# Optimization experiments

Hardware: AMD Instinct MI355X
Metric: run time of the kernel (lower is better)

Reference implementation:

```python
import jax, jax.numpy as jnp
import numpy as np

N_SRC, N_DST, E, D, H = 100000, 10000, 320000, 128, 128
LN_EPS = 1e-5


def setup_inputs() -> dict:
    key = jax.random.key(0)
    ks = jax.random.split(key, 12)
    h_src = jax.random.normal(ks[0], (N_SRC, D), jnp.float32)
    h_dst = jax.random.normal(ks[1], (N_DST, D), jnp.float32)
    s_emb = jax.random.normal(ks[2], (N_DST, D), jnp.float32)
    edge_weight = jax.random.uniform(ks[3], (E,), jnp.float32)
    src_idx = jax.random.randint(ks[4], (E,), 0, N_SRC)
    dst_idx = jnp.sort(jax.random.randint(ks[5], (E,), 0, N_DST))
    # session_attention: Linear(2D->H, no bias) -> tanh -> Linear(H->1, no bias)
    W1 = jax.random.normal(ks[6], (2 * D, H), jnp.float32) / np.sqrt(2 * D)
    w2 = jax.random.normal(ks[7], (H,), jnp.float32) / np.sqrt(H)
    # output_proj: Linear(2D->D) with bias
    Wo = jax.random.normal(ks[8], (2 * D, D), jnp.float32) / np.sqrt(2 * D)
    bo = jnp.zeros((D,), jnp.float32)
    gamma = jnp.ones((D,), jnp.float32)
    beta = jnp.zeros((D,), jnp.float32)
    return {"h_src": h_src, "h_dst": h_dst, "s_emb": s_emb,
            "edge_weight": edge_weight, "src_idx": src_idx, "dst_idx": dst_idx,
            "W1": W1, "w2": w2, "Wo": Wo, "bo": bo, "gamma": gamma, "beta": beta}


def reference(h_src, h_dst, s_emb, edge_weight, src_idx, dst_idx, W1, w2, Wo, bo, gamma, beta):
    d = h_src.shape[1]
    # concat([h_src[src], s_emb[dst]]) @ W1 == h_src[src] @ W1[:d] + s_emb[dst] @ W1[d:]
    # project per-node first (cheaper than per-edge concat matmul)
    p_src = h_src @ W1[:d]          # [N_src, H]
    p_dst = s_emb @ W1[d:]          # [N_dst, H]
    raw = jnp.tanh(p_src[src_idx] + p_dst[dst_idx]) @ w2   # [E]
    raw = raw * edge_weight
    # edge_softmax: segment softmax over incoming edges of each dst node
    seg_max = jax.ops.segment_max(raw, dst_idx, num_segments=h_dst.shape[0])
    seg_max = jnp.where(jnp.isfinite(seg_max), seg_max, 0.0)  # handle degree-0 dsts
    ex = jnp.exp(raw - seg_max[dst_idx])
    den = jax.ops.segment_sum(ex, dst_idx, num_segments=h_dst.shape[0])
    attn = ex / den[dst_idx]                                 # [E]
    # u_mul_e + sum: weighted gather-scatter aggregation
    h_global = jax.ops.segment_sum(h_src[src_idx] * attn[:, None], dst_idx,
                                   num_segments=h_dst.shape[0])  # [N_dst, D]
    # output_proj on concat([h_dst, h_global])
    out = h_dst @ Wo[:d] + h_global @ Wo[d:] + bo
    # residual + layer norm (dropout = identity in eval)
    x = h_dst + out
    mu = jnp.mean(x, axis=-1, keepdims=True)
    var = jnp.mean((x - mu) ** 2, axis=-1, keepdims=True)
    y = (x - mu) / jnp.sqrt(var + LN_EPS) * gamma + beta
    return (y, attn[:, None])
```

## Files before the change

### kernel.cpp

```cpp
#include <hip/hip_runtime.h>
#include <math.h>

#define D128 128
#define SCAPW 256

typedef unsigned int uint32;
typedef unsigned short ushort_t;
typedef short bf16x8 __attribute__((ext_vector_type(8)));
typedef float f32x4 __attribute__((ext_vector_type(4)));
typedef float f32x2 __attribute__((ext_vector_type(2)));

__device__ __forceinline__ ushort_t bf16_of(float x) {
  uint32 u = __float_as_uint(x);
  return (ushort_t)((u + 0x7fffu + ((u >> 16) & 1u)) >> 16);
}
__device__ __forceinline__ uint32 pack_bf2(float x, float y) {
  uint32 bx = __float_as_uint(x);
  uint32 by = __float_as_uint(y);
  bx = (bx + 0x7fffu + ((bx >> 16) & 1u)) >> 16;
  by = (by + 0x7fffu + ((by >> 16) & 1u)) & 0xffff0000u;
  return bx | by;
}

__device__ __forceinline__ float fast_tanh(float x) {
  float e = __expf(2.0f * x);
  float r = __builtin_amdgcn_rcpf(1.0f + e);
  return fmaf(-2.0f, r, 1.0f);
}

__device__ __forceinline__ uint32 pack_fp8x4(float a, float b, float c, float d) {
  int u = __builtin_amdgcn_cvt_pk_fp8_f32(a, b, 0, false);
  u = __builtin_amdgcn_cvt_pk_fp8_f32(c, d, u, true);
  return (uint32)u;
}

__device__ __forceinline__ bf16x8 bf16x8_of(float4 a, float4 c) {
  union { uint4 u; bf16x8 h; } r;
  r.u.x = pack_bf2(a.x, a.y);
  r.u.y = pack_bf2(a.z, a.w);
  r.u.z = pack_bf2(c.x, c.y);
  r.u.w = pack_bf2(c.z, c.w);
  return r.h;
}

__global__ __launch_bounds__(256) void prep_all(
    const float* __restrict__ W1, const float* __restrict__ Wo,
    const int* __restrict__ dst_idx,
    ushort_t* __restrict__ Wfrag, ushort_t* __restrict__ Wo_frag,
    int* __restrict__ off, int E, int N) {
  const int b = blockIdx.x;
  const int tid = threadIdx.x;
  if (b < 16) {
    int t = b * 256 + tid;
    int lane = t & 63;
    int kc = (t >> 6) & 3;
    int nt = (t >> 8) & 7;
    int h = (t >> 11) & 1;
    int m = lane & 15;
    int quad = lane >> 4;
    int krow = h * D128 + kc * 32 + quad * 8;
    int ncol = nt * 16 + m;
    ushort_t fr[8];
#pragma unroll
    for (int j = 0; j < 8; j++) fr[j] = bf16_of(W1[(size_t)(krow + j) * D128 + ncol]);
    *(uint4*)(Wfrag + (size_t)t * 8) = *(const uint4*)fr;
  } else if (b < 32) {
    int t = (b - 16) * 256 + tid;
    int lane = t & 63;
    int kc = (t >> 6) & 7;
    int nt = (t >> 9) & 7;
    int m = lane & 15;
    int quad = lane >> 4;
    int krow = kc * 32 + quad * 8;
    int ncol = nt * 16 + m;
    ushort_t fr[8];
#pragma unroll
    for (int j = 0; j < 8; j++) fr[j] = bf16_of(Wo[(size_t)(krow + j) * D128 + ncol]);
    *(uint4*)(Wo_frag + (size_t)t * 8) = *(const uint4*)fr;
  } else {
    int e = (b - 32) * 256 + tid;
    if (e >= E) return;
    int d = dst_idx[e];
    int dprev = (e == 0) ? -1 : dst_idx[e - 1];
    for (int v = dprev + 1; v <= d; v++) off[v] = e;
    if (e == E - 1) {
      for (int v = d + 1; v <= N; v++) off[v] = E;
    }
  }
}

__global__ __launch_bounds__(256) void gemm_mfma(
    const float* __restrict__ Xa, const float* __restrict__ Xb,
    const ushort_t* __restrict__ Wfrag,
    uint32* __restrict__ Pa, uint32* __restrict__ Pb,
    uint32* __restrict__ x_f8,
    int Ma, int Mb, int nblk_a) {
  __shared__ uint32 Ys8[128][36];
  const int blk = blockIdx.x;
  const float* X;
  const bf16x8* Wf;
  uint32* P;
  int M, row0;
  bool emit8;
  if (blk < nblk_a) {
    X = Xa; P = Pa; Wf = (const bf16x8*)Wfrag;           M = Ma; row0 = blk * 128; emit8 = true;
  } else {
    X = Xb; P = Pb; Wf = (const bf16x8*)(Wfrag + 16384); M = Mb; row0 = (blk - nblk_a) * 128; emit8 = false;
  }

  const int tid = threadIdx.x;
  const int wave = tid >> 6;
  const int lane = tid & 63;
  const int m = lane & 15;
  const int quad = lane >> 4;

  const int ra0 = min(row0 + wave * 32 + m, M - 1);
  const int ra1 = min(row0 + wave * 32 + 16 + m, M - 1);

  f32x4 acc[2][8];
#pragma unroll
  for (int st = 0; st < 2; st++)
#pragma unroll
    for (int nt = 0; nt < 8; nt++) acc[st][nt] = (f32x4){0.f, 0.f, 0.f, 0.f};

#pragma unroll
  for (int kc = 0; kc < 4; kc++) {
    const float* p0 = X + (size_t)ra0 * D128 + kc * 32 + quad * 8;
    const float* p1 = X + (size_t)ra1 * D128 + kc * 32 + quad * 8;
    float4 a0 = *(const float4*)p0;
    float4 a1 = *(const float4*)(p0 + 4);
    float4 b0 = *(const float4*)p1;
    float4 b1 = *(const float4*)(p1 + 4);
    bf16x8 x0 = bf16x8_of(a0, a1);
    bf16x8 x1 = bf16x8_of(b0, b1);
    if (emit8) {
      uint2 q;
      q.x = pack_fp8x4(a0.x, a0.y, a0.z, a0.w);
      q.y = pack_fp8x4(a1.x, a1.y, a1.z, a1.w);
      *(uint2*)(x_f8 + (size_t)ra0 * 32 + kc * 8 + quad * 2) = q;
      q.x = pack_fp8x4(b0.x, b0.y, b0.z, b0.w);
      q.y = pack_fp8x4(b1.x, b1.y, b1.z, b1.w);
      *(uint2*)(x_f8 + (size_t)ra1 * 32 + kc * 8 + quad * 2) = q;
    }
#pragma unroll
    for (int nt = 0; nt < 8; nt++) {
      bf16x8 wf = Wf[(nt * 4 + kc) * 64 + lane];
      acc[0][nt] = __builtin_amdgcn_mfma_f32_16x16x32_bf16(wf, x0, acc[0][nt], 0, 0, 0);
      acc[1][nt] = __builtin_amdgcn_mfma_f32_16x16x32_bf16(wf, x1, acc[1][nt], 0, 0, 0);
    }
  }

#pragma unroll
  for (int st = 0; st < 2; st++)
#pragma unroll
    for (int nt = 0; nt < 8; nt++)
      Ys8[wave * 32 + st * 16 + m][nt * 4 + quad] =
          pack_fp8x4(acc[st][nt][0], acc[st][nt][1], acc[st][nt][2], acc[st][nt][3]);
  __syncthreads();

#pragma unroll
  for (int it = 0; it < 4; it++) {
    int f = tid + 256 * it;
    int row = f >> 3;
    int cu = (f & 7) * 4;
    int grow = row0 + row;
    if (grow < M) *(uint4*)(P + (size_t)grow * 32 + cu) = *(const uint4*)(&Ys8[row][cu]);
  }
}

__global__ __launch_bounds__(256) void attn_agg_kernel(
    const uint32* __restrict__ p_src_f8, const uint32* __restrict__ p_dst_f8,
    const float* __restrict__ w2, const float* __restrict__ ew,
    const int* __restrict__ src_idx, const int* __restrict__ off,
    const uint32* __restrict__ h_src_f8,
    float* __restrict__ attn_out, uint32* __restrict__ h_glob_bf, int N_dst) {
  const int tid = threadIdx.x;
  const int wv = tid >> 6;
  const int lane = tid & 63;
  const int v = blockIdx.x * 4 + wv;

  __shared__ float sex[4][SCAPW];
  __shared__ int ssrc[4][SCAPW];
  if (v >= N_dst) return;

  const int lo = off[v], hi = off[v + 1];
  const int deg = hi - lo;
  const int sub = lane & 15;
  const int eg = lane >> 4;
  const bool fast = (deg <= SCAPW);

  float4 wA = *(const float4*)(w2 + sub * 8);
  float4 wB = *(const float4*)(w2 + sub * 8 + 4);
  uint2 pdu = *(const uint2*)(p_dst_f8 + (size_t)v * 32 + sub * 2);
  f32x2 pd0 = __builtin_amdgcn_cvt_pk_f32_fp8(pdu.x, false);
  f32x2 pd1 = __builtin_amdgcn_cvt_pk_f32_fp8(pdu.x, true);
  f32x2 pd2 = __builtin_amdgcn_cvt_pk_f32_fp8(pdu.y, false);
  f32x2 pd3 = __builtin_amdgcn_cvt_pk_f32_fp8(pdu.y, true);

  float den = 0.f;
  for (int base = 0; base < deg; base += 4) {
    const int ei = base + eg;
    float ex = 0.f;
    if (ei < deg) {
      const int e = lo + ei;
      const int s = src_idx[e];
      const float ewv = ew[e];
      uint2 us = *(const uint2*)(p_src_f8 + (size_t)s * 32 + sub * 2);
      f32x2 a0 = __builtin_amdgcn_cvt_pk_f32_fp8(us.x, false);
      f32x2 a1 = __builtin_amdgcn_cvt_pk_f32_fp8(us.x, true);
      f32x2 a2 = __builtin_amdgcn_cvt_pk_f32_fp8(us.y, false);
      f32x2 a3 = __builtin_amdgcn_cvt_pk_f32_fp8(us.y, true);
      float sc;
      sc = fast_tanh(a0.x + pd0.x) * wA.x;
      sc = fmaf(fast_tanh(a0.y + pd0.y), wA.y, sc);
      sc = fmaf(fast_tanh(a1.x + pd1.x), wA.z, sc);
      sc = fmaf(fast_tanh(a1.y + pd1.y), wA.w, sc);
      sc = fmaf(fast_tanh(a2.x + pd2.x), wB.x, sc);
      sc = fmaf(fast_tanh(a2.y + pd2.y), wB.y, sc);
      sc = fmaf(fast_tanh(a3.x + pd3.x), wB.z, sc);
      sc = fmaf(fast_tanh(a3.y + pd3.y), wB.w, sc);
#pragma unroll
      for (int o = 1; o <= 8; o <<= 1) sc += __shfl_xor(sc, o, 64);
      ex = __expf(sc * ewv);
      if (sub == 0) {
        if (fast) { sex[wv][ei] = ex; ssrc[wv][ei] = s; }
        else attn_out[lo + ei] = ex;
      }
    }
    den += (sub == 0) ? ex : 0.f;
  }
#pragma unroll
  for (int o = 1; o <= 32; o <<= 1) den += __shfl_xor(den, o, 64);
  const float inv = (deg > 0) ? 1.0f / den : 0.0f;

  const int c4 = lane & 31;
  const int hw = lane >> 5;
  float a0 = 0.f, a1 = 0.f, a2 = 0.f, a3 = 0.f;

  if (fast) {
    const int pad = (deg + 15) & ~15;
    for (int i = deg + lane; i < pad; i += 64) { sex[wv][i] = 0.f; ssrc[wv][i] = 0; }
    for (int i = lane; i < deg; i += 64) attn_out[lo + i] = sex[wv][i] * inv;
    for (int b = 0; b < pad; b += 16) {
#pragma unroll
      for (int j = 0; j < 8; j++) {
        const int idx = b + j * 2 + hw;
        float ex = sex[wv][idx];
        int s = ssrc[wv][idx];
        uint32 u = h_src_f8[(size_t)s * 32 + c4];
        f32x2 h0 = __builtin_amdgcn_cvt_pk_f32_fp8(u, false);
        f32x2 h1 = __builtin_amdgcn_cvt_pk_f32_fp8(u, true);
        a0 = fmaf(ex, h0.x, a0);
        a1 = fmaf(ex, h0.y, a1);
        a2 = fmaf(ex, h1.x, a2);
        a3 = fmaf(ex, h1.y, a3);
      }
    }
  } else {
    for (int b = 0; b < deg; b += 16) {
#pragma unroll
      for (int j = 0; j < 8; j++) {
        const int idx = b + j * 2 + hw;
        float ex = 0.f;
        int s = 0;
        if (idx < deg) { ex = attn_out[lo + idx]; s = src_idx[lo + idx]; }
        uint32 u = h_src_f8[(size_t)s * 32 + c4];
        f32x2 h0 = __builtin_amdgcn_cvt_pk_f32_fp8(u, false);
        f32x2 h1 = __builtin_amdgcn_cvt_pk_f32_fp8(u, true);
        a0 = fmaf(ex, h0.x, a0);
        a1 = fmaf(ex, h0.y, a1);
        a2 = fmaf(ex, h1.x, a2);
        a3 = fmaf(ex, h1.y, a3);
      }
    }
    for (int i = lane; i < deg; i += 64) attn_out[lo + i] *= inv;
  }

  a0 += __shfl_xor(a0, 32, 64);
  a1 += __shfl_xor(a1, 32, 64);
  a2 += __shfl_xor(a2, 32, 64);
  a3 += __shfl_xor(a3, 32, 64);
  if (hw == 0) {
    uint2 o;
    o.x = pack_bf2(a0 * inv, a1 * inv);
    o.y = pack_bf2(a2 * inv, a3 * inv);
    *(uint2*)(h_glob_bf + (size_t)v * 64 + c4 * 2) = o;
  }
}

__global__ __launch_bounds__(128) void out_mfma_ln(
    const float* __restrict__ h_dst, const ushort_t* __restrict__ h_glob_bf,
    const ushort_t* __restrict__ Wo_frag,
    const float* __restrict__ bo,
    const float* __restrict__ gamma, const float* __restrict__ beta,
    float* __restrict__ y, int N) {
  __shared__ float sbo[128], sgam[128], sbet[128];
  const int tid = threadIdx.x;
  if (tid < 128) { sbo[tid] = bo[tid]; sgam[tid] = gamma[tid]; sbet[tid] = beta[tid]; }
  __syncthreads();

  const int w = tid >> 6;
  const int lane = tid & 63;
  const int m = lane & 15;
  const int quad = lane >> 4;
  const int row0 = blockIdx.x * 32 + w * 16;
  const int ra = min(row0 + m, N - 1);
  const bf16x8* Wf = (const bf16x8*)Wo_frag;

  f32x4 acc[8];
#pragma unroll
  for (int nt = 0; nt < 8; nt++) acc[nt] = (f32x4){0.f, 0.f, 0.f, 0.f};

#pragma unroll
  for (int kc = 0; kc < 8; kc++) {
    bf16x8 a;
    if (kc < 4) {
      const float* p = h_dst + (size_t)ra * D128 + kc * 32 + quad * 8;
      float4 f0 = *(const float4*)p;
      float4 f1 = *(const float4*)(p + 4);
      a = bf16x8_of(f0, f1);
    } else {
      a = *(const bf16x8*)(h_glob_bf + (size_t)ra * D128 + (kc & 3) * 32 + quad * 8);
    }
#pragma unroll
    for (int nt = 0; nt < 8; nt++) {
      bf16x8 bfr = Wf[(nt * 8 + kc) * 64 + lane];
      acc[nt] = __builtin_amdgcn_mfma_f32_16x16x32_bf16(a, bfr, acc[nt], 0, 0, 0);
    }
  }

#pragma unroll
  for (int r = 0; r < 4; r++) {
    const int grow = row0 + quad * 4 + r;
    const int gr = min(grow, N - 1);
    float x[8];
    float s1 = 0.f, s2 = 0.f;
#pragma unroll
    for (int nt = 0; nt < 8; nt++) {
      float hd = h_dst[(size_t)gr * D128 + nt * 16 + m];
      float xv = hd + acc[nt][r] + sbo[nt * 16 + m];
      x[nt] = xv;
      s1 += xv;
      s2 = fmaf(xv, xv, s2);
    }
#pragma unroll
    for (int o = 1; o <= 8; o <<= 1) {
      s1 += __shfl_xor(s1, o, 64);
      s2 += __shfl_xor(s2, o, 64);
    }
    float mu = s1 * (1.0f / 128.0f);
    float var = s2 * (1.0f / 128.0f) - mu * mu;
    float rstd = __builtin_amdgcn_rcpf(sqrtf(var + 1e-5f));
    if (grow < N) {
#pragma unroll
      for (int nt = 0; nt < 8; nt++) {
        int c = nt * 16 + m;
        y[(size_t)grow * D128 + c] = (x[nt] - mu) * rstd * sgam[c] + sbet[c];
      }
    }
  }
}

extern "C" void kernel_launch(void* const* d_in, const int* in_sizes, int n_in,
                              void* d_out, int out_size, void* d_ws, size_t ws_size,
                              hipStream_t stream) {
  const float* h_src = (const float*)d_in[0];
  const float* h_dst = (const float*)d_in[1];
  const float* s_emb = (const float*)d_in[2];
  const float* ew    = (const float*)d_in[3];
  const int* src_idx = (const int*)d_in[4];
  const int* dst_idx = (const int*)d_in[5];
  const float* W1    = (const float*)d_in[6];
  const float* w2    = (const float*)d_in[7];
  const float* Wo    = (const float*)d_in[8];
  const float* bo    = (const float*)d_in[9];
  const float* gamma = (const float*)d_in[10];
  const float* beta  = (const float*)d_in[11];

  const int N_src = in_sizes[0] / D128;
  const int N_dst = in_sizes[1] / D128;
  const int E = in_sizes[3];

  float* out_y = (float*)d_out;
  float* out_attn = out_y + (size_t)N_dst * D128;

  uint32* p_src_f8 = (uint32*)d_ws;
  uint32* p_dst_f8 = p_src_f8 + (size_t)N_src * 32;
  uint32* h_src_f8 = p_dst_f8 + (size_t)N_dst * 32;
  uint32* h_glob_bf = h_src_f8 + (size_t)N_src * 32;
  int* seg_off = (int*)(h_glob_bf + (size_t)N_dst * 64);
  ushort_t* Wfrag = (ushort_t*)(seg_off + N_dst + 1 + 3);
  ushort_t* Wo_frag = Wfrag + 32768;

  const int nblk_a = (N_src + 127) / 128;
  const int nblk_b = (N_dst + 127) / 128;
  const int nb_seg = (E + 255) / 256;

  prep_all<<<32 + nb_seg, 256, 0, stream>>>(
      W1, Wo, dst_idx, Wfrag, Wo_frag, seg_off, E, N_dst);
  gemm_mfma<<<nblk_a + nblk_b, 256, 0, stream>>>(
      h_src, s_emb, Wfrag, p_src_f8, p_dst_f8, h_src_f8, N_src, N_dst, nblk_a);
  attn_agg_kernel<<<(N_dst + 3) / 4, 256, 0, stream>>>(
      p_src_f8, p_dst_f8, w2, ew, src_idx, seg_off, h_src_f8, out_attn,
      h_glob_bf, N_dst);
  out_mfma_ln<<<(N_dst + 31) / 32, 128, 0, stream>>>(
      h_dst, (const ushort_t*)h_glob_bf, Wo_frag,
      bo, gamma, beta, out_y, N_dst);
}
```

Measured before the change: 172.6 us.

## Halve GEMM row tile to 64 and prefetch all input rows up front

The node-projection GEMM now gives each wave 16 rows instead of 32, so a block covers 64 rows and twice as many blocks launch. All eight float4 loads of each row are issued before any MFMA work, so more memory requests are in flight per wave. In exchange, each W1 fragment load from L2 feeds only one MFMA instead of two, which roughly doubles weight-fragment traffic per output row.

```diff
diff --git a/kernel.cpp b/kernel.cpp
--- a/kernel.cpp
+++ b/kernel.cpp
@@ -95,7 +95,7 @@
     uint32* __restrict__ Pa, uint32* __restrict__ Pb,
     uint32* __restrict__ x_f8,
     int Ma, int Mb, int nblk_a) {
-  __shared__ uint32 Ys8[128][36];
+  __shared__ uint32 Ys8[64][36];
   const int blk = blockIdx.x;
   const float* X;
   const bf16x8* Wf;
@@ -103,9 +103,9 @@
   int M, row0;
   bool emit8;
   if (blk < nblk_a) {
-    X = Xa; P = Pa; Wf = (const bf16x8*)Wfrag;           M = Ma; row0 = blk * 128; emit8 = true;
+    X = Xa; P = Pa; Wf = (const bf16x8*)Wfrag;           M = Ma; row0 = blk * 64; emit8 = true;
   } else {
-    X = Xb; P = Pb; Wf = (const bf16x8*)(Wfrag + 16384); M = Mb; row0 = (blk - nblk_a) * 128; emit8 = false;
+    X = Xb; P = Pb; Wf = (const bf16x8*)(Wfrag + 16384); M = Mb; row0 = (blk - nblk_a) * 64; emit8 = false;
   }
 
   const int tid = threadIdx.x;
@@ -114,52 +114,44 @@
   const int m = lane & 15;
   const int quad = lane >> 4;
 
-  const int ra0 = min(row0 + wave * 32 + m, M - 1);
-  const int ra1 = min(row0 + wave * 32 + 16 + m, M - 1);
-
-  f32x4 acc[2][8];
-#pragma unroll
-  for (int st = 0; st < 2; st++)
-#pragma unroll
-    for (int nt = 0; nt < 8; nt++) acc[st][nt] = (f32x4){0.f, 0.f, 0.f, 0.f};
-
+  const int ra = min(row0 + wave * 16 + m, M - 1);
+  const float* xp = X + (size_t)ra * D128 + quad * 8;
+
+  float4 xf[8];
 #pragma unroll
   for (int kc = 0; kc < 4; kc++) {
-    const float* p0 = X + (size_t)ra0 * D128 + kc * 32 + quad * 8;
-    const float* p1 = X + (size_t)ra1 * D128 + kc * 32 + quad * 8;
-    float4 a0 = *(const float4*)p0;
-    float4 a1 = *(const float4*)(p0 + 4);
-    float4 b0 = *(const float4*)p1;
-    float4 b1 = *(const float4*)(p1 + 4);
-    bf16x8 x0 = bf16x8_of(a0, a1);
-    bf16x8 x1 = bf16x8_of(b0, b1);
+    xf[kc * 2]     = *(const float4*)(xp + kc * 32);
+    xf[kc * 2 + 1] = *(const float4*)(xp + kc * 32 + 4);
+  }
+
+  f32x4 acc[8];
+#pragma unroll
+  for (int nt = 0; nt < 8; nt++) acc[nt] = (f32x4){0.f, 0.f, 0.f, 0.f};
+
+#pragma unroll
+  for (int kc = 0; kc < 4; kc++) {
+    bf16x8 x0 = bf16x8_of(xf[kc * 2], xf[kc * 2 + 1]);
     if (emit8) {
       uint2 q;
-      q.x = pack_fp8x4(a0.x, a0.y, a0.z, a0.w);
-      q.y = pack_fp8x4(a1.x, a1.y, a1.z, a1.w);
-      *(uint2*)(x_f8 + (size_t)ra0 * 32 + kc * 8 + quad * 2) = q;
-      q.x = pack_fp8x4(b0.x, b0.y, b0.z, b0.w);
-      q.y = pack_fp8x4(b1.x, b1.y, b1.z, b1.w);
-      *(uint2*)(x_f8 + (size_t)ra1 * 32 + kc * 8 + quad * 2) = q;
+      q.x = pack_fp8x4(xf[kc * 2].x, xf[kc * 2].y, xf[kc * 2].z, xf[kc * 2].w);
+      q.y = pack_fp8x4(xf[kc * 2 + 1].x, xf[kc * 2 + 1].y, xf[kc * 2 + 1].z, xf[kc * 2 + 1].w);
+      *(uint2*)(x_f8 + (size_t)ra * 32 + kc * 8 + quad * 2) = q;
     }
 #pragma unroll
     for (int nt = 0; nt < 8; nt++) {
       bf16x8 wf = Wf[(nt * 4 + kc) * 64 + lane];
-      acc[0][nt] = __builtin_amdgcn_mfma_f32_16x16x32_bf16(wf, x0, acc[0][nt], 0, 0, 0);
-      acc[1][nt] = __builtin_amdgcn_mfma_f32_16x16x32_bf16(wf, x1, acc[1][nt], 0, 0, 0);
-    }
-  }
-
-#pragma unroll
-  for (int st = 0; st < 2; st++)
-#pragma unroll
-    for (int nt = 0; nt < 8; nt++)
-      Ys8[wave * 32 + st * 16 + m][nt * 4 + quad] =
-          pack_fp8x4(acc[st][nt][0], acc[st][nt][1], acc[st][nt][2], acc[st][nt][3]);
+      acc[nt] = __builtin_amdgcn_mfma_f32_16x16x32_bf16(wf, x0, acc[nt], 0, 0, 0);
+    }
+  }
+
+#pragma unroll
+  for (int nt = 0; nt < 8; nt++)
+    Ys8[wave * 16 + m][nt * 4 + quad] =
+        pack_fp8x4(acc[nt][0], acc[nt][1], acc[nt][2], acc[nt][3]);
   __syncthreads();
 
 #pragma unroll
-  for (int it = 0; it < 4; it++) {
+  for (int it = 0; it < 2; it++) {
     int f = tid + 256 * it;
     int row = f >> 3;
     int cu = (f & 7) * 4;
@@ -392,8 +384,8 @@
   ushort_t* Wfrag = (ushort_t*)(seg_off + N_dst + 1 + 3);
   ushort_t* Wo_frag = Wfrag + 32768;
 
-  const int nblk_a = (N_src + 127) / 128;
-  const int nblk_b = (N_dst + 127) / 128;
+  const int nblk_a = (N_src + 63) / 64;
+  const int nblk_b = (N_dst + 63) / 64;
   const int nb_seg = (E + 255) / 256;
 
   prep_all<<<32 + nb_seg, 256, 0, stream>>>(
```

After: 165.4 us. 1.04x faster.
